# Performance work log

Measured on AMD Instinct MI355X. Metric: run time of the kernel, lower is better.

## Reference

```python
import jax, jax.numpy as jnp
import numpy as np

B, C_IN, C_OUT, STYLE, H, W = 4, 128, 128, 512, 64, 64
C_QK = C_OUT // 8
EPS = 1e-5


def setup_inputs() -> dict:
    key = jax.random.key(0)
    ks = jax.random.split(key, 16)
    n = jax.random.normal
    return {
        "x": n(ks[0], (B, C_IN, H, W), jnp.float32),
        "style": n(ks[1], (B, STYLE), jnp.float32),
        "conv_w": n(ks[2], (C_OUT, C_IN, 3, 3), jnp.float32) * 0.02,
        "conv_b": jnp.zeros((C_OUT,), jnp.float32),
        "ss_w": n(ks[3], (C_OUT, STYLE), jnp.float32) * 0.02,
        "ss_b": jnp.zeros((C_OUT,), jnp.float32),
        "sb_w": n(ks[4], (C_OUT, STYLE), jnp.float32) * 0.02,
        "sb_b": jnp.zeros((C_OUT,), jnp.float32),
        "q_w": n(ks[5], (C_QK, C_OUT, 1, 1), jnp.float32) * 0.02,
        "q_b": jnp.zeros((C_QK,), jnp.float32),
        "k_w": n(ks[6], (C_QK, C_OUT, 1, 1), jnp.float32) * 0.02,
        "k_b": jnp.zeros((C_QK,), jnp.float32),
        "v_w": n(ks[7], (C_OUT, C_OUT, 1, 1), jnp.float32) * 0.02,
        "v_b": jnp.zeros((C_OUT,), jnp.float32),
        "gamma": jnp.zeros((1,), jnp.float32),
    }


def _conv3x3(x, w, b):
    y = jax.lax.conv_general_dilated(
        x, w, window_strides=(1, 1), padding=((1, 1), (1, 1)),
        dimension_numbers=("NCHW", "OIHW", "NCHW"))
    return y + b[None, :, None, None]


def _conv1x1(x, w, b):
    # w: [O, I, 1, 1] -> pointwise channel mix
    y = jnp.einsum("bihw,oi->bohw", x, w[:, :, 0, 0])
    return y + b[None, :, None, None]


def reference(x, style, conv_w, conv_b, ss_w, ss_b, sb_w, sb_b,
              q_w, q_b, k_w, k_b, v_w, v_b, gamma):
    # conv + AdaIN-style modulation
    h = _conv3x3(x, conv_w, conv_b)                       # [B,C,H,W]
    scale = (style @ ss_w.T + ss_b)[:, :, None, None]
    bias = (style @ sb_w.T + sb_b)[:, :, None, None]
    h = h * (1.0 + scale) + bias

    # self-attention over spatial positions (no sqrt(d) scaling)
    b, c, hh, ww = h.shape
    n = hh * ww
    q = _conv1x1(h, q_w, q_b).reshape(b, -1, n)           # [B,Cqk,N]
    k = _conv1x1(h, k_w, k_b).reshape(b, -1, n)           # [B,Cqk,N]
    v = _conv1x1(h, v_w, v_b).reshape(b, c, n)            # [B,C,N]
    attn = jnp.einsum("bcq,bck->bqk", q, k)               # [B,N,N]
    attn = jax.nn.softmax(attn, axis=-1)
    out = jnp.einsum("bcm,bnm->bcn", v, attn).reshape(b, c, hh, ww)
    h = gamma[0] * out + h

    # InstanceNorm (affine=False), biased variance, eps=1e-5
    mu = jnp.mean(h, axis=(2, 3), keepdims=True)
    var = jnp.var(h, axis=(2, 3), keepdims=True)
    h = (h - mu) * jax.lax.rsqrt(var + EPS)

    # LeakyReLU(0.2)
    return jnp.where(h >= 0, h, 0.2 * h)
```

## Files before the change

### kernel.cpp

```cpp
#include <hip/hip_runtime.h>
#include <hip/hip_bf16.h>
#include <math.h>

#define NN 4096
#define EPSV 1e-5f

typedef short short8 __attribute__((ext_vector_type(8)));
typedef float f32x4 __attribute__((ext_vector_type(4)));

static constexpr size_t OFF_SCALE = 0;
static constexpr size_t OFF_BIAS  = 512;
static constexpr size_t OFF_H     = 1024;
static constexpr size_t OFF_Q     = OFF_H  + (size_t)4*128*4096;
static constexpr size_t OFF_K     = OFF_Q  + (size_t)4*16*4096;
static constexpr size_t OFF_V     = OFF_K  + (size_t)4*16*4096;
static constexpr size_t OFF_AO    = OFF_V  + (size_t)4*128*4096;
static constexpr size_t OFF_XHI   = OFF_AO + (size_t)4*128*4096;
static constexpr size_t OFF_XLO   = OFF_XHI + (size_t)4*66*66*128/2;
static constexpr size_t OFF_WPK   = OFF_XLO + (size_t)4*66*66*128/2;

__device__ __forceinline__ unsigned short f2bf(float f) {
    unsigned u = __float_as_uint(f);
    unsigned r = u + 0x7FFFu + ((u >> 16) & 1u);
    return (unsigned short)(r >> 16);
}
__device__ __forceinline__ float bf2f(unsigned short h) {
    return __uint_as_float(((unsigned)h) << 16);
}

__global__ __launch_bounds__(256)
void prep(const float* __restrict__ x, const float* __restrict__ conv_w,
          const float* __restrict__ style,
          const float* __restrict__ ss_w, const float* __restrict__ ss_b,
          const float* __restrict__ sb_w, const float* __restrict__ sb_b,
          float* __restrict__ ws) {
    const int bi = blockIdx.x;
    const int t  = threadIdx.x;

    if (bi < 528) {
        const int yp = bi >> 3;
        const int b  = (bi & 7) >> 1;
        const int h  = bi & 1;
        unsigned short* xh = (unsigned short*)(ws + OFF_XHI) + ((size_t)b * 66 + yp) * 66 * 128;
        unsigned short* xl = (unsigned short*)(ws + OFF_XLO) + ((size_t)b * 66 + yp) * 66 * 128;
        const short8 z8 = {0,0,0,0,0,0,0,0};

        if (yp == 0 || yp == 65) {
            for (int task = t; task < 1056; task += 256) {
                const int buf = task >= 528;
                const int tt  = task - 528 * buf;
                const int xp  = tt >> 3, g = tt & 7;
                unsigned short* p = (buf ? xl : xh) + (size_t)xp * 128 + h * 64 + g * 8;
                *(short8*)p = z8;
            }
            return;
        }
        const int y = yp - 1;
        __shared__ float s[64][65];
        const float* src = x + (size_t)b * 128 * NN + (size_t)h * 64 * NN + y * 64;
        for (int j = t; j < 4096; j += 256) {
            const int ci = j >> 6, xx = j & 63;
            s[xx][ci] = src[(size_t)ci * NN + xx];
        }
        if (t < 32) {
            const int buf = t >> 4, e = (t >> 3) & 1, g = t & 7;
            unsigned short* p = (buf ? xl : xh) + (size_t)e * 65 * 128 + h * 64 + g * 8;
            *(short8*)p = z8;
        }
        __syncthreads();
        #pragma unroll
        for (int rep = 0; rep < 2; ++rep) {
            const int task = t + rep * 256;
            const int xx = task >> 3, g = task & 7;
            short8 vh, vl;
            #pragma unroll
            for (int j = 0; j < 8; ++j) {
                const float f = s[xx][g * 8 + j];
                const unsigned short hh = f2bf(f);
                vh[j] = (short)hh;
                vl[j] = (short)f2bf(f - bf2f(hh));
            }
            const size_t o = (size_t)(xx + 1) * 128 + h * 64 + g * 8;
            *(short8*)(xh + o) = vh;
            *(short8*)(xl + o) = vl;
        }
    } else if (bi < 672) {
        const int id = (bi - 528) * 4 + (t >> 6);
        const int l  = t & 63;
        const int cog = id & 7;
        const int q   = id >> 3;
        const int tap = q % 9;
        const int p2  = q / 9;
        const int kb  = p2 & 3;
        const int part= p2 >> 2;
        const int co  = cog * 16 + (l & 15);
        const int ci0 = kb * 32 + (l >> 4) * 8;
        short8 v;
        #pragma unroll
        for (int j = 0; j < 8; ++j) {
            const float f = conv_w[(size_t)co * 1152 + (size_t)(ci0 + j) * 9 + tap];
            const unsigned short hh = f2bf(f);
            v[j] = (short)(part == 0 ? hh : f2bf(f - bf2f(hh)));
        }
        unsigned short* wp = (unsigned short*)(ws + OFF_WPK);
        *(short8*)(wp + ((size_t)id * 64 + l) * 8) = v;
    } else {
        const int bc = (bi - 672) * 4 + (t >> 6);
        const int b = bc >> 7, c = bc & 127;
        const int lane = t & 63;
        const float* st = style + (size_t)b * 512;
        float s1 = 0.f, s2 = 0.f;
        for (int e = lane; e < 512; e += 64) {
            const float sv = st[e];
            s1 = fmaf(sv, ss_w[(size_t)c * 512 + e], s1);
            s2 = fmaf(sv, sb_w[(size_t)c * 512 + e], s2);
        }
        #pragma unroll
        for (int off = 32; off; off >>= 1) {
            s1 += __shfl_xor(s1, off);
            s2 += __shfl_xor(s2, off);
        }
        if (lane == 0) {
            ws[OFF_SCALE + bc] = s1 + ss_b[c];
            ws[OFF_BIAS  + bc] = s2 + sb_b[c];
        }
    }
}

struct St { short8 ah0, ah1, al0, al1, bh0, bh1, bl0, bl1; };

__global__ __launch_bounds__(256, 2)
void mfma_conv(float* __restrict__ ws, const float* __restrict__ conv_b) {
    const int y   = blockIdx.x;
    const int coh = blockIdx.y;
    const int b   = blockIdx.z;
    const int t   = threadIdx.x;
    const int l   = t & 63;
    const int wv  = t >> 6;
    const int wm  = wv & 1;
    const int wn  = wv >> 1;
    const int x0  = wm * 32;
    const int cobase = coh * 64 + wn * 32;
    const int lr = l & 15, lg = l >> 4;

    const unsigned short* xh = (const unsigned short*)(ws + OFF_XHI) + (size_t)b * 66 * 66 * 128;
    const unsigned short* xl = (const unsigned short*)(ws + OFF_XLO) + (size_t)b * 66 * 66 * 128;
    const unsigned short* wp = (const unsigned short*)(ws + OFF_WPK);

    const size_t aL0 = (size_t)(x0 + lr) * 128 + (size_t)lg * 8;
    const size_t aL1 = aL0 + 16 * 128;
    const int cog0 = coh * 4 + wn * 2;

    f32x4 acc00 = {0,0,0,0}, acc01 = {0,0,0,0};
    f32x4 acc10 = {0,0,0,0}, acc11 = {0,0,0,0};

    auto load_st = [&](St& S, int s) {
        const int kb  = s / 9;
        const int tap = s - 9 * kb;
        const int ky  = tap / 3;
        const int kx  = tap - 3 * ky;
        const size_t su = ((size_t)(y + ky) * 66 + kx) * 128 + (size_t)kb * 32;
        const unsigned short* ph = xh + su;
        const unsigned short* pl = xl + su;
        S.ah0 = *(const short8*)(ph + aL0);
        S.ah1 = *(const short8*)(ph + aL1);
        S.al0 = *(const short8*)(pl + aL0);
        S.al1 = *(const short8*)(pl + aL1);
        const unsigned short* pbh = wp + ((size_t)(kb * 9 + tap) * 8 + cog0) * 512 + (size_t)l * 8;
        const unsigned short* pbl = pbh + (size_t)36 * 8 * 512;
        S.bh0 = *(const short8*)pbh;
        S.bh1 = *(const short8*)(pbh + 512);
        S.bl0 = *(const short8*)pbl;
        S.bl1 = *(const short8*)(pbl + 512);
    };
    auto do_mfma = [&](const St& S) {
        acc00 = __builtin_amdgcn_mfma_f32_16x16x32_bf16(S.ah0, S.bh0, acc00, 0,0,0);
        acc01 = __builtin_amdgcn_mfma_f32_16x16x32_bf16(S.ah0, S.bh1, acc01, 0,0,0);
        acc10 = __builtin_amdgcn_mfma_f32_16x16x32_bf16(S.ah1, S.bh0, acc10, 0,0,0);
        acc11 = __builtin_amdgcn_mfma_f32_16x16x32_bf16(S.ah1, S.bh1, acc11, 0,0,0);
        acc00 = __builtin_amdgcn_mfma_f32_16x16x32_bf16(S.al0, S.bh0, acc00, 0,0,0);
        acc01 = __builtin_amdgcn_mfma_f32_16x16x32_bf16(S.al0, S.bh1, acc01, 0,0,0);
        acc10 = __builtin_amdgcn_mfma_f32_16x16x32_bf16(S.al1, S.bh0, acc10, 0,0,0);
        acc11 = __builtin_amdgcn_mfma_f32_16x16x32_bf16(S.al1, S.bh1, acc11, 0,0,0);
        acc00 = __builtin_amdgcn_mfma_f32_16x16x32_bf16(S.ah0, S.bl0, acc00, 0,0,0);
        acc01 = __builtin_amdgcn_mfma_f32_16x16x32_bf16(S.ah0, S.bl1, acc01, 0,0,0);
        acc10 = __builtin_amdgcn_mfma_f32_16x16x32_bf16(S.ah1, S.bl0, acc10, 0,0,0);
        acc11 = __builtin_amdgcn_mfma_f32_16x16x32_bf16(S.ah1, S.bl1, acc11, 0,0,0);
    };

    St SA, SB, SC;
    load_st(SA, 0); load_st(SB, 1); load_st(SC, 2);
    for (int s = 0; s < 33; s += 3) {
        do_mfma(SA); load_st(SA, s + 3);
        do_mfma(SB); load_st(SB, s + 4);
        do_mfma(SC); load_st(SC, s + 5);
    }
    do_mfma(SA); do_mfma(SB); do_mfma(SC);

    const float* scp = ws + OFF_SCALE + b * 128;
    const float* bip = ws + OFF_BIAS  + b * 128;
    float* hout = ws + OFF_H;
    #pragma unroll
    for (int nf = 0; nf < 2; ++nf) {
        const int co = cobase + nf * 16 + lr;
        const float sc = 1.f + scp[co];
        const float bi = bip[co];
        const float cb = conv_b[co];
        #pragma unroll
        for (int mf = 0; mf < 2; ++mf) {
            f32x4 a = (nf == 0) ? (mf == 0 ? acc00 : acc10)
                                : (mf == 0 ? acc01 : acc11);
            float4 o;
            o.x = (a[0] + cb) * sc + bi;
            o.y = (a[1] + cb) * sc + bi;
            o.z = (a[2] + cb) * sc + bi;
            o.w = (a[3] + cb) * sc + bi;
            const int xo = x0 + mf * 16 + lg * 4;
            *(float4*)(hout + (size_t)(b * 128 + co) * NN + y * 64 + xo) = o;
        }
    }
}

__global__ __launch_bounds__(256)
void qkv_kernel(float* __restrict__ ws,
                const float* __restrict__ qw, const float* __restrict__ qb,
                const float* __restrict__ kw, const float* __restrict__ kb,
                const float* __restrict__ vw, const float* __restrict__ vb,
                const float* __restrict__ gamma) {
    if (gamma[0] == 0.f) return;
    const int b  = blockIdx.y;
    const int oc = blockIdx.x;
    const float* wrow; float bias; float* dst;
    if (oc < 16)      { wrow = qw + (size_t)oc * 128;        bias = qb[oc];
                        dst = ws + OFF_Q + (size_t)(b * 16 + oc) * NN; }
    else if (oc < 32) { int c = oc - 16; wrow = kw + (size_t)c * 128; bias = kb[c];
                        dst = ws + OFF_K + (size_t)(b * 16 + c) * NN; }
    else              { int c = oc - 32; wrow = vw + (size_t)c * 128; bias = vb[c];
                        dst = ws + OFF_V + (size_t)(b * 128 + c) * NN; }
    const float* hb = ws + OFF_H + (size_t)b * 128 * NN;
    for (int n = threadIdx.x; n < NN; n += 256) {
        float a = bias;
        for (int ci = 0; ci < 128; ++ci) a += hb[(size_t)ci * NN + n] * wrow[ci];
        dst[n] = a;
    }
}

__global__ __launch_bounds__(256)
void attn_kernel(float* __restrict__ ws, const float* __restrict__ gamma) {
    if (gamma[0] == 0.f) return;
    const int b  = blockIdx.y;
    const int n0 = blockIdx.x * 64;
    const int t  = threadIdx.x;

    __shared__ float q_s[16][64];
    __shared__ float k_s[16][64];
    __shared__ float v_s[64][129];
    __shared__ float p_s[64][65];
    __shared__ float m_run[64], l_run[64], sc_s[64];

    const float* qp = ws + OFF_Q + (size_t)b * 16 * NN;
    const float* kp = ws + OFF_K + (size_t)b * 16 * NN;
    const float* vp = ws + OFF_V + (size_t)b * 128 * NN;

    for (int idx = t; idx < 16 * 64; idx += 256) {
        int cq = idx >> 6, j = idx & 63;
        q_s[cq][j] = qp[(size_t)cq * NN + n0 + j];
    }
    if (t < 64) { m_run[t] = -1e30f; l_run[t] = 0.f; }

    const int n  = t & 63;
    const int cg = t >> 6;
    float acc[32];
    #pragma unroll
    for (int i = 0; i < 32; ++i) acc[i] = 0.f;
    __syncthreads();

    for (int mt = 0; mt < 64; ++mt) {
        const int m0 = mt * 64;
        for (int idx = t; idx < 16 * 64; idx += 256) {
            int cq = idx >> 6, j = idx & 63;
            k_s[cq][j] = kp[(size_t)cq * NN + m0 + j];
        }
        for (int idx = t; idx < 128 * 64; idx += 256) {
            int c = idx >> 6, j = idx & 63;
            v_s[j][c] = vp[(size_t)c * NN + m0 + j];
        }
        __syncthreads();
        {
            const int nn2   = t & 63;
            const int mbase = (t >> 6) * 16;
            for (int mi = 0; mi < 16; ++mi) {
                const int mm = mbase + mi;
                float s = 0.f;
                #pragma unroll
                for (int cq = 0; cq < 16; ++cq) s += q_s[cq][nn2] * k_s[cq][mm];
                p_s[nn2][mm] = s;
            }
        }
        __syncthreads();
        if (t < 64) {
            float mold = m_run[t];
            float mx = mold;
            for (int mm = 0; mm < 64; ++mm) mx = fmaxf(mx, p_s[t][mm]);
            float sc = expf(mold - mx);
            float rs = 0.f;
            for (int mm = 0; mm < 64; ++mm) {
                float p = expf(p_s[t][mm] - mx);
                p_s[t][mm] = p;
                rs += p;
            }
            l_run[t] = l_run[t] * sc + rs;
            m_run[t] = mx;
            sc_s[t]  = sc;
        }
        __syncthreads();
        {
            const float sc = sc_s[n];
            #pragma unroll
            for (int i = 0; i < 32; ++i) acc[i] *= sc;
            for (int mm = 0; mm < 64; ++mm) {
                const float p = p_s[n][mm];
                #pragma unroll
                for (int i = 0; i < 32; ++i) acc[i] += p * v_s[mm][cg * 32 + i];
            }
        }
        __syncthreads();
    }

    const float inv = 1.f / l_run[n];
    float* ao = ws + OFF_AO + (size_t)b * 128 * NN;
    for (int i = 0; i < 32; ++i)
        ao[(size_t)(cg * 32 + i) * NN + n0 + n] = acc[i] * inv;
}

__global__ __launch_bounds__(256)
void inorm_lrelu(const float* __restrict__ ws,
                 const float* __restrict__ gamma,
                 float* __restrict__ out) {
    const int bc = blockIdx.x;
    const int t  = threadIdx.x;
    const float g = gamma[0];

    const float4* hp = (const float4*)(ws + OFF_H  + (size_t)bc * NN);
    const float4* ap = (const float4*)(ws + OFF_AO + (size_t)bc * NN);

    float4 v[4];
    #pragma unroll
    for (int i = 0; i < 4; ++i) {
        float4 hv = hp[t + 256 * i];
        if (g != 0.f) {
            float4 av = ap[t + 256 * i];
            hv.x += g * av.x; hv.y += g * av.y; hv.z += g * av.z; hv.w += g * av.w;
        }
        v[i] = hv;
    }

    float s1 = 0.f, s2 = 0.f;
    #pragma unroll
    for (int i = 0; i < 4; ++i) {
        s1 += v[i].x + v[i].y + v[i].z + v[i].w;
        s2 += v[i].x * v[i].x + v[i].y * v[i].y + v[i].z * v[i].z + v[i].w * v[i].w;
    }
    #pragma unroll
    for (int off = 32; off; off >>= 1) {
        s1 += __shfl_xor(s1, off);
        s2 += __shfl_xor(s2, off);
    }
    __shared__ float r1[4], r2[4];
    if ((t & 63) == 0) { r1[t >> 6] = s1; r2[t >> 6] = s2; }
    __syncthreads();
    const float S1 = r1[0] + r1[1] + r1[2] + r1[3];
    const float S2 = r2[0] + r2[1] + r2[2] + r2[3];
    const float mu  = S1 * (1.f / 4096.f);
    const float var = S2 * (1.f / 4096.f) - mu * mu;
    const float rs  = 1.f / sqrtf(var + EPSV);

    float4* op = (float4*)out + (size_t)bc * (NN / 4);
    #pragma unroll
    for (int i = 0; i < 4; ++i) {
        float4 o;
        o.x = (v[i].x - mu) * rs; o.x = o.x >= 0.f ? o.x : 0.2f * o.x;
        o.y = (v[i].y - mu) * rs; o.y = o.y >= 0.f ? o.y : 0.2f * o.y;
        o.z = (v[i].z - mu) * rs; o.z = o.z >= 0.f ? o.z : 0.2f * o.z;
        o.w = (v[i].w - mu) * rs; o.w = o.w >= 0.f ? o.w : 0.2f * o.w;
        op[t + 256 * i] = o;
    }
}

extern "C" void kernel_launch(void* const* d_in, const int* in_sizes, int n_in,
                              void* d_out, int out_size, void* d_ws, size_t ws_size,
                              hipStream_t stream) {
    const float* x      = (const float*)d_in[0];
    const float* style  = (const float*)d_in[1];
    const float* conv_w = (const float*)d_in[2];
    const float* conv_b = (const float*)d_in[3];
    const float* ss_w   = (const float*)d_in[4];
    const float* ss_b   = (const float*)d_in[5];
    const float* sb_w   = (const float*)d_in[6];
    const float* sb_b   = (const float*)d_in[7];
    const float* q_w    = (const float*)d_in[8];
    const float* q_b    = (const float*)d_in[9];
    const float* k_w    = (const float*)d_in[10];
    const float* k_b    = (const float*)d_in[11];
    const float* v_w    = (const float*)d_in[12];
    const float* v_b    = (const float*)d_in[13];
    const float* gamma  = (const float*)d_in[14];
    float* ws  = (float*)d_ws;
    float* out = (float*)d_out;

    prep<<<800, 256, 0, stream>>>(x, conv_w, style, ss_w, ss_b, sb_w, sb_b, ws);
    mfma_conv<<<dim3(64, 2, 4), 256, 0, stream>>>(ws, conv_b);
    qkv_kernel<<<dim3(160, 4), 256, 0, stream>>>(ws, q_w, q_b, k_w, k_b, v_w, v_b, gamma);
    attn_kernel<<<dim3(64, 4), 256, 0, stream>>>(ws, gamma);
    inorm_lrelu<<<512, 256, 0, stream>>>(ws, gamma, out);
}
```

Before: 141.4 us.

## Split conv K dimension across two wave groups with LDS reduction

The 3x3 conv MFMA kernel now launches 512 threads per block. Two groups of four waves each handle half of the input channels, and the partial accumulators are combined through shared memory before the epilogue. The software pipeline also deepens from three to six in-flight stages. This aims to double the waves per block and shorten each wave's serial MFMA chain, which should hide load latency better. The costs are more registers per thread, an LDS round trip with a barrier, and possible occupancy limits.

```diff
diff --git a/kernel.cpp b/kernel.cpp
--- a/kernel.cpp
+++ b/kernel.cpp
@@ -129,7 +129,7 @@
 
 struct St { short8 ah0, ah1, al0, al1, bh0, bh1, bl0, bl1; };
 
-__global__ __launch_bounds__(256, 2)
+__global__ __launch_bounds__(512, 2)
 void mfma_conv(float* __restrict__ ws, const float* __restrict__ conv_b) {
     const int y   = blockIdx.x;
     const int coh = blockIdx.y;
@@ -137,37 +137,42 @@
     const int t   = threadIdx.x;
     const int l   = t & 63;
     const int wv  = t >> 6;
-    const int wm  = wv & 1;
-    const int wn  = wv >> 1;
+    const int wsub = wv & 3;
+    const int khalf = wv >> 2;
+    const int wm  = wsub & 1;
+    const int wn  = wsub >> 1;
     const int x0  = wm * 32;
     const int cobase = coh * 64 + wn * 32;
     const int lr = l & 15, lg = l >> 4;
 
-    const unsigned short* xh = (const unsigned short*)(ws + OFF_XHI) + (size_t)b * 66 * 66 * 128;
-    const unsigned short* xl = (const unsigned short*)(ws + OFF_XLO) + (size_t)b * 66 * 66 * 128;
-    const unsigned short* wp = (const unsigned short*)(ws + OFF_WPK);
+    __shared__ float s_red[4][4][4][64];
+
+    const unsigned short* xh = (const unsigned short*)(ws + OFF_XHI)
+                             + (size_t)b * 66 * 66 * 128 + (size_t)khalf * 64;
+    const unsigned short* xl = (const unsigned short*)(ws + OFF_XLO)
+                             + (size_t)b * 66 * 66 * 128 + (size_t)khalf * 64;
+    const unsigned short* wpb = (const unsigned short*)(ws + OFF_WPK)
+                              + ((size_t)(khalf * 18) * 8 + (coh * 4 + wn * 2)) * 512
+                              + (size_t)l * 8;
 
     const size_t aL0 = (size_t)(x0 + lr) * 128 + (size_t)lg * 8;
     const size_t aL1 = aL0 + 16 * 128;
-    const int cog0 = coh * 4 + wn * 2;
 
     f32x4 acc00 = {0,0,0,0}, acc01 = {0,0,0,0};
     f32x4 acc10 = {0,0,0,0}, acc11 = {0,0,0,0};
 
     auto load_st = [&](St& S, int s) {
-        const int kb  = s / 9;
-        const int tap = s - 9 * kb;
+        const int kbl = s / 9;
+        const int tap = s - 9 * kbl;
         const int ky  = tap / 3;
         const int kx  = tap - 3 * ky;
-        const size_t su = ((size_t)(y + ky) * 66 + kx) * 128 + (size_t)kb * 32;
-        const unsigned short* ph = xh + su;
-        const unsigned short* pl = xl + su;
-        S.ah0 = *(const short8*)(ph + aL0);
-        S.ah1 = *(const short8*)(ph + aL1);
-        S.al0 = *(const short8*)(pl + aL0);
-        S.al1 = *(const short8*)(pl + aL1);
-        const unsigned short* pbh = wp + ((size_t)(kb * 9 + tap) * 8 + cog0) * 512 + (size_t)l * 8;
-        const unsigned short* pbl = pbh + (size_t)36 * 8 * 512;
+        const size_t su = ((size_t)(y + ky) * 66 + kx) * 128 + (size_t)kbl * 32;
+        S.ah0 = *(const short8*)(xh + su + aL0);
+        S.ah1 = *(const short8*)(xh + su + aL1);
+        S.al0 = *(const short8*)(xl + su + aL0);
+        S.al1 = *(const short8*)(xl + su + aL1);
+        const unsigned short* pbh = wpb + (size_t)s * 4096;
+        const unsigned short* pbl = pbh + (size_t)36 * 4096;
         S.bh0 = *(const short8*)pbh;
         S.bh1 = *(const short8*)(pbh + 512);
         S.bl0 = *(const short8*)pbl;
@@ -188,14 +193,35 @@
         acc11 = __builtin_amdgcn_mfma_f32_16x16x32_bf16(S.ah1, S.bl1, acc11, 0,0,0);
     };
 
-    St SA, SB, SC;
-    load_st(SA, 0); load_st(SB, 1); load_st(SC, 2);
-    for (int s = 0; s < 33; s += 3) {
-        do_mfma(SA); load_st(SA, s + 3);
-        do_mfma(SB); load_st(SB, s + 4);
-        do_mfma(SC); load_st(SC, s + 5);
-    }
-    do_mfma(SA); do_mfma(SB); do_mfma(SC);
+    St S[6];
+    #pragma unroll
+    for (int i = 0; i < 6; ++i) load_st(S[i], i);
+    #pragma unroll
+    for (int ss = 6; ss < 18; ss += 6) {
+        #pragma unroll
+        for (int i = 0; i < 6; ++i) { do_mfma(S[i]); load_st(S[i], ss + i); }
+    }
+    #pragma unroll
+    for (int i = 0; i < 6; ++i) do_mfma(S[i]);
+
+    if (khalf == 1) {
+        #pragma unroll
+        for (int e = 0; e < 4; ++e) {
+            s_red[wsub][0][e][l] = acc00[e];
+            s_red[wsub][1][e][l] = acc01[e];
+            s_red[wsub][2][e][l] = acc10[e];
+            s_red[wsub][3][e][l] = acc11[e];
+        }
+    }
+    __syncthreads();
+    if (khalf == 1) return;
+    #pragma unroll
+    for (int e = 0; e < 4; ++e) {
+        acc00[e] += s_red[wsub][0][e][l];
+        acc01[e] += s_red[wsub][1][e][l];
+        acc10[e] += s_red[wsub][2][e][l];
+        acc11[e] += s_red[wsub][3][e][l];
+    }
 
     const float* scp = ws + OFF_SCALE + b * 128;
     const float* bip = ws + OFF_BIAS  + b * 128;
@@ -409,7 +435,7 @@
     float* out = (float*)d_out;
 
     prep<<<800, 256, 0, stream>>>(x, conv_w, style, ss_w, ss_b, sb_w, sb_b, ws);
-    mfma_conv<<<dim3(64, 2, 4), 256, 0, stream>>>(ws, conv_b);
+    mfma_conv<<<dim3(64, 2, 4), 512, 0, stream>>>(ws, conv_b);
     qkv_kernel<<<dim3(160, 4), 256, 0, stream>>>(ws, q_w, q_b, k_w, k_b, v_w, v_b, gamma);
     attn_kernel<<<dim3(64, 4), 256, 0, stream>>>(ws, gamma);
     inorm_lrelu<<<512, 256, 0, stream>>>(ws, gamma, out);
```

Result: no change. 141.6 us (+0.1%).
